# Optimization experiments

Measured on AMD Instinct MI355X. Metric: run time of the kernel, lower is better.

Reference implementation:

```python
import jax, jax.numpy as jnp
import numpy as np

B, C, H, W = 8, 6, 512, 512
N_SIGMA = 1
NUM_CLASS = 3
RES = 256
FG_W = 1.0
MAX_ID = 16  # instance ids in [0, 16); 0 is background
W_INST, W_VAR, W_SEED = 1.0, 10.0, 1.0
GAMMA = 2.0


def make_xym():
    ym = jnp.broadcast_to(jnp.linspace(0.0, H // RES, H)[None, :, None], (1, H, W))
    xm = jnp.broadcast_to(jnp.linspace(0.0, W // RES, W)[None, None, :], (1, H, W))
    return jnp.concatenate([xm, ym], 0)  # (2, H, W), channel 0 = x, 1 = y


def lovasz_hinge_flat(logits, labels_f):
    # logits, labels_f: (P,) ; labels in {0,1}
    signs = 2.0 * labels_f - 1.0
    errors = 1.0 - logits * signs
    order = jnp.argsort(-errors)  # descending
    errors_sorted = errors[order]
    gt_sorted = labels_f[order]
    gts = gt_sorted.sum()
    intersection = gts - jnp.cumsum(gt_sorted)
    union = gts + jnp.cumsum(1.0 - gt_sorted)
    jaccard = 1.0 - intersection / union
    grad = jaccard.at[1:].set(jaccard[1:] - jaccard[:-1])
    grad = jax.lax.stop_gradient(grad)
    return jnp.sum(jax.nn.relu(errors_sorted) * grad)


def focal_loss_multiclass(logits, target):
    # logits: (B, NUM_CLASS, H, W), target: (B, H, W) int class ids
    logpt = jax.nn.log_softmax(logits, axis=1)
    lp = jnp.take_along_axis(logpt, target[:, None], axis=1)[:, 0]  # (B,H,W)
    pt = jnp.exp(lp)
    return jnp.mean(-((1.0 - pt) ** GAMMA) * lp)


def setup_inputs() -> dict:
    key = jax.random.key(0)
    k1, k2, k3 = jax.random.split(key, 3)
    prediction = jax.random.normal(k1, (B, C, H, W), dtype=jnp.float32)
    labels = jax.random.randint(k2, (B, NUM_CLASS, H, W), 0, 2, dtype=jnp.int32)
    instances = jax.random.randint(k3, (B, 1, H, W), 0, MAX_ID, dtype=jnp.int32)
    return {"prediction": prediction, "labels": labels, "instances": instances}


def _loss(prediction, labels, instances):
    xym = make_xym()
    ids = jnp.arange(1, MAX_ID)

    def per_image(pred_b, inst_b, lab_b):
        spatial_emb = jnp.tanh(pred_b[0:2]) + xym           # (2,H,W)
        sigma = pred_b[2]                                    # (H,W), n_sigma=1
        seed = jax.nn.sigmoid(pred_b[2 + N_SIGMA + NUM_CLASS - 1])  # (H,W)
        label_fg = lab_b[-1]                                 # (H,W)
        bg_seed = jnp.sum(jnp.where(label_fg == 0, seed ** 2, 0.0))

        def per_id(k):
            mask = (inst_b[0] == k).astype(pred_b.dtype)     # (H,W)
            cnt = mask.sum()
            safe = jnp.maximum(cnt, 1.0)
            center = (xym * mask).sum((1, 2)) / safe         # (2,) to_center=True
            s_mean = (sigma * mask).sum() / safe
            var = (mask * (sigma - jax.lax.stop_gradient(s_mean)) ** 2).sum() / safe
            s = jnp.exp(s_mean * 10.0)
            dist = jnp.exp(-s * ((spatial_emb - center[:, None, None]) ** 2).sum(0))
            lov = lovasz_hinge_flat((dist * 2.0 - 1.0).ravel(), mask.ravel())
            seed_fg = FG_W * (mask * (seed - jax.lax.stop_gradient(dist)) ** 2).sum()
            return cnt > 0, lov, var, seed_fg

        valid, lov, var, sfg = jax.vmap(per_id)(ids)
        nobj = jnp.maximum(valid.sum().astype(pred_b.dtype), 1.0)
        inst_loss = jnp.where(valid, lov, 0.0).sum() / nobj
        var_loss = jnp.where(valid, var, 0.0).sum() / nobj
        seed_loss = (bg_seed + jnp.where(valid, sfg, 0.0).sum()) / (H * W)
        return W_INST * inst_loss + W_VAR * var_loss + W_SEED * seed_loss

    per_b = jax.vmap(per_image)(prediction, instances, labels)
    binary_closs = focal_loss_multiclass(
        prediction[:, 2 + N_SIGMA:2 + N_SIGMA + NUM_CLASS],
        jnp.argmax(labels, axis=1))
    return jnp.mean(per_b) + binary_closs


def reference(prediction, labels, instances):
    return _loss(prediction, labels, instances)
```

## Files before the change

kernel.cpp:

```cpp
#include <hip/hip_runtime.h>
#include <math.h>

#define BB 8
#define HWH (512*512)
#define NID 15
#define NSEG (BB*NID)
#define NBINS 256
#define AAF ((float)NBINS/13.0f)
#define LOG2E 1.442695041f
#define LN2 0.6931471806f
#define SLICES 128

typedef unsigned int uint32;
typedef unsigned long long uint64;

__device__ __forceinline__ float ftanh(float x){
    float t = __expf(2.0f*x);
    return 1.0f - 2.0f*__builtin_amdgcn_rcpf(t + 1.0f);
}
__device__ __forceinline__ float fsigmoid(float x){
    return __builtin_amdgcn_rcpf(1.0f + __expf(-x));
}
__device__ __forceinline__ float sconst(float x){
    return __uint_as_float(__builtin_amdgcn_readfirstlane(__float_as_uint(x)));
}

__global__ __launch_bounds__(256, 8) void phase1f(const float* __restrict__ pred,
        const int* __restrict__ labels, const int* __restrict__ inst,
        uint64* __restrict__ pstat64, float* __restrict__ pstatf,
        float* __restrict__ pstatf2,
        float* __restrict__ bgseed_p, float* __restrict__ focal_p){
    int blk = blockIdx.x;
    int b = blk >> 8;
    int t = threadIdx.x;
    int q = (blk & 255)*256 + t;

    __shared__ uint64 s64[NID];
    __shared__ float ssig[NID], ssig2[NID];
    __shared__ float wfb[4][2];
    if (t < NID){ s64[t] = 0ull; ssig[t] = 0.0f; ssig2[t] = 0.0f; }
    __syncthreads();

    const int Q = HWH/4;
    const float4* P = (const float4*)(pred + (size_t)b*6*HWH);
    const int4* L = (const int4*)(labels + (size_t)b*3*HWH);
    const int4* I = (const int4*)(inst + (size_t)b*HWH);
    float4 sg4 = P[2*Q+q], z3 = P[3*Q+q], z4 = P[4*Q+q], z5 = P[5*Q+q];
    int4 id4 = I[q];
    int4 l0 = L[q], l1 = L[Q+q], l2 = L[2*Q+q];
    int p = q*4;
    int w0 = p & 511, h0 = p >> 9;

    float facc = 0.0f, bacc = 0.0f;
    auto px = [&](float sgv, float z3v, float z4v, float z5v, int id,
                  int L0, int L1, int L2, int wv){
        float seed = fsigmoid(z5v);
        if (L2 == 0) bacc += seed*seed;
        int tc = 0, best = L0;
        if (L1 > best){ tc = 1; best = L1; }
        if (L2 > best){ tc = 2; }
        float m = fmaxf(z3v, fmaxf(z4v, z5v));
        float e3 = __expf(z3v-m), e4 = __expf(z4v-m), e5 = __expf(z5v-m);
        float sum = e3+e4+e5;
        float lse = m + __logf(sum);
        float zt = (tc==0) ? z3v : ((tc==1) ? z4v : z5v);
        float et = (tc==0) ? e3  : ((tc==1) ? e4  : e5);
        float lp = zt - lse;
        float pt = et*__builtin_amdgcn_rcpf(sum);
        float om = 1.0f - pt;
        facc -= om*om*lp;
        if (id > 0){
            atomicAdd(&s64[id-1],
                      (1ull<<42) | ((uint64)(uint32)wv<<21) | (uint64)(uint32)h0);
            atomicAdd(&ssig[id-1], sgv);
            atomicAdd(&ssig2[id-1], sgv*sgv);
        }
    };
    px(sg4.x, z3.x, z4.x, z5.x, id4.x, l0.x, l1.x, l2.x, w0);
    px(sg4.y, z3.y, z4.y, z5.y, id4.y, l0.y, l1.y, l2.y, w0+1);
    px(sg4.z, z3.z, z4.z, z5.z, id4.z, l0.z, l1.z, l2.z, w0+2);
    px(sg4.w, z3.w, z4.w, z5.w, id4.w, l0.w, l1.w, l2.w, w0+3);

    for (int o = 32; o; o >>= 1){
        facc += __shfl_xor(facc, o);
        bacc += __shfl_xor(bacc, o);
    }
    if ((t & 63) == 0){ wfb[t>>6][0] = facc; wfb[t>>6][1] = bacc; }
    __syncthreads();
    if (t < NID){
        pstat64[blk*16 + t] = s64[t];
        pstatf [blk*16 + t] = ssig[t];
        pstatf2[blk*16 + t] = ssig2[t];
    }
    if (t == 0){
        focal_p[blk]  = wfb[0][0]+wfb[1][0]+wfb[2][0]+wfb[3][0];
        bgseed_p[blk] = wfb[0][1]+wfb[1][1]+wfb[2][1]+wfb[3][1];
    }
}

__global__ __launch_bounds__(512) void phaseR(const uint64* __restrict__ pstat64,
        const float* __restrict__ pstatf, const float* __restrict__ pstatf2,
        const float* __restrict__ focal_p, const float* __restrict__ bgseed_p,
        float* __restrict__ stats, float* __restrict__ derived,
        float* __restrict__ results,
        float* __restrict__ focalR, float* __restrict__ bgseedR,
        uint32* __restrict__ Hzero, float* __restrict__ part2f){
    int b = blockIdx.x;
    int t = threadIdx.x;

    {
        const int stripe = 2*NSEG*NBINS/8;
        for (int i = b*stripe + t; i < (b+1)*stripe; i += 512) Hzero[i] = 0u;
        if (b == 0 && t < NSEG) part2f[t] = 0.0f;
    }

    int k = t & 15, chunk = t >> 4;
    float acnt = 0, asw = 0, ash = 0, af = 0, af2 = 0;
    for (int i = 0; i < 8; i++){
        int blk = b*256 + chunk*8 + i;
        uint64 v = pstat64[blk*16 + k];
        acnt += (float)(uint32)(v >> 42);
        asw  += (float)(uint32)((v >> 21) & 0x1FFFFF);
        ash  += (float)(uint32)(v & 0x1FFFFF);
        af   += pstatf[blk*16 + k];
        af2  += pstatf2[blk*16 + k];
    }
    __shared__ float tc[16], tw[16], th[16], ts[16], ts2[16];
    if (t < 16){ tc[t]=0; tw[t]=0; th[t]=0; ts[t]=0; ts2[t]=0; }
    __syncthreads();
    atomicAdd(&tc[k], acnt);
    atomicAdd(&tw[k], asw);
    atomicAdd(&th[k], ash);
    atomicAdd(&ts[k], af);
    atomicAdd(&ts2[k], af2);
    __syncthreads();
    if (t < NID){
        float cnt = tc[t];
        float safe = fmaxf(cnt, 1.0f);
        float inv = 1.0f/safe;
        const float SC = 2.0f/511.0f;
        derived[(b*NID+t)*4+0] = tw[t]*SC*inv;
        derived[(b*NID+t)*4+1] = th[t]*SC*inv;
        float sm = ts[t]*inv;
        derived[(b*NID+t)*4+2] = __expf(10.0f*sm);
        derived[(b*NID+t)*4+3] = sm;
        stats[b*60 + t*4] = cnt;
        results[(size_t)(b*NID+t)*3 + 1] = ts2[t] - cnt*sm*sm;
    }
    int w = t >> 6, lane = t & 63;
    if (w == 0){
        float f = 0;
        for (int j = 0; j < 4; j++) f += focal_p[b*256 + j*64 + lane];
        for (int o = 32; o; o >>= 1) f += __shfl_xor(f, o);
        if (lane == 0) focalR[b] = f;
    } else if (w == 1){
        float g = 0;
        for (int j = 0; j < 4; j++) g += bgseed_p[b*256 + j*64 + lane];
        for (int o = 32; o; o >>= 1) g += __shfl_xor(g, o);
        if (lane == 0) bgseedR[b] = g;
    }
}

__global__ __launch_bounds__(512, 8) void phaseLH(const float* __restrict__ pred,
        const int* __restrict__ inst, const float* __restrict__ derived,
        uint32* __restrict__ Hc, uint32* __restrict__ Hg,
        float* __restrict__ part2f){
    int idx = blockIdx.x;
    int b = idx & 7;
    int sp = idx >> 3;
    int t = threadIdx.x;
    int lane = t & 63;

    __shared__ __align__(16) uint32 hist[NID*NBINS];
    __shared__ float ssl[NID];
    __shared__ float vsB[NID];
    {
        uint4* hz = (uint4*)hist;
        for (int i = t; i < NID*NBINS/4; i += 512) hz[i] = make_uint4(0,0,0,0);
    }
    if (t < NID){
        ssl[t] = derived[(size_t)(b*NID + t)*4 + 2];
        vsB[t] = 0.0f;
    }
    float kcx[NID], kcy[NID], kcs[NID];
    #pragma unroll
    for (int j = 0; j < NID; j++){
        const float* d0 = derived + (size_t)(b*NID + j)*4;
        kcx[j] = sconst(d0[0]);
        kcy[j] = sconst(d0[1]);
        kcs[j] = sconst(LOG2E*AAF*d0[2]);
    }
    __syncthreads();

    const int Q = HWH/4;
    const int qps = Q / SLICES;
    int q0 = sp * qps;
    const float* pb = pred + (size_t)b*6*HWH;
    const float4* P0 = (const float4*)pb;
    const float4* P1 = P0 + Q;
    const float* z5p = pb + 5*HWH;
    const int4* I = (const int4*)(inst + (size_t)b*HWH);
    const float SC = 2.0f/511.0f;

    for (int q = q0 + t; q < q0 + qps; q += 512){
        int4 id4 = I[q];
        float4 a = P0[q], c = P1[q];
        int p = q*4;
        float gx = (float)(p & 511)*SC;
        float gy = (float)(p >> 9)*SC;
        auto px = [&](float av, float cv, int id, float gxv, int pi){
            float ex = ftanh(av) + gxv;
            float ey = ftanh(cv) + gy;
            int own = id - 1;
            float r2own = 0.0f;
            #pragma unroll
            for (int j = 0; j < NID; j++){
                float dx = ex - kcx[j], dy = ey - kcy[j];
                float r2 = fmaf(dx, dx, dy*dy);
                if (j == own) r2own = r2;
                float binf = fmaf(-kcs[j], r2, (float)NBINS);
                binf = fminf(fmaxf(binf, 0.0f), (float)(NBINS-1));
                int bin = (int)binf;
                bool isown = (j == own);
                bool hot = (bin == 0) && !isown;
                uint64 bal = __ballot(hot);
                if (hot){
                    if ((bal & ((1ull << lane) - 1ull)) == 0ull)
                        atomicAdd(&hist[j*NBINS],
                                  ((uint32)__popcll(bal)) << 16);
                } else if (!isown){
                    atomicAdd(&hist[j*NBINS + bin], 65536u);
                }
            }
            if (own >= 0){
                float d = __expf(-ssl[own]*r2own);
                float e = fmaf(-2.0f, d, 2.0f);
                float bf = fmaf(__log2f(e), AAF, (float)NBINS - AAF);
                bf = fminf(fmaxf(bf, 0.0f), (float)(NBINS-1));
                atomicAdd(&hist[own*NBINS + (int)bf], 65537u);
                float seed = fsigmoid(z5p[pi]);
                float sd = seed - d;
                atomicAdd(&vsB[own], sd*sd);
            }
        };
        px(a.x, c.x, id4.x, gx,      p);
        px(a.y, c.y, id4.y, gx+SC,   p+1);
        px(a.z, c.z, id4.z, gx+2*SC, p+2);
        px(a.w, c.w, id4.w, gx+3*SC, p+3);
    }
    __syncthreads();
    size_t base = (size_t)b*NID*NBINS;
    for (int i = t; i < NID*NBINS; i += 512){
        uint32 v = hist[i];
        if (v){
            uint32 cc = v >> 16, gg = v & 0xFFFFu;
            if (cc) atomicAdd(&Hc[base + i], cc);
            if (gg) atomicAdd(&Hg[base + i], gg);
        }
    }
    if (t < NID && vsB[t] != 0.0f)
        atomicAdd(&part2f[b*NID + t], vsB[t]);
}

__global__ __launch_bounds__(256) void phaseLS(const uint32* __restrict__ Hc,
        const uint32* __restrict__ Hg, const float* __restrict__ part2f,
        const float* __restrict__ stats, float* __restrict__ results){
    int idx = blockIdx.x;
    int b = idx & 7, k = idx >> 3;
    int seg = b*NID + k;
    int t = threadIdx.x;

    __shared__ uint32 wbc[4], wbg[4], wexc[4], wexg[4];
    __shared__ float wsum[4];

    size_t base = (size_t)seg*NBINS;
    uint32 cd = Hc[base + NBINS-1-t];
    uint32 gd = Hg[base + NBINS-1-t];
    uint32 ci = cd, gi2 = gd;
    int lane = t & 63, w = t >> 6;
    for (int o = 1; o < 64; o <<= 1){
        uint32 cu = __shfl_up(ci, o);
        uint32 gu = __shfl_up(gi2, o);
        if (lane >= o){ ci += cu; gi2 += gu; }
    }
    if (lane == 63){ wbc[w] = ci; wbg[w] = gi2; }
    __syncthreads();
    if (t == 0){
        uint32 rc = 0, rg = 0;
        for (int i = 0; i < 4; i++){
            uint32 a = wbc[i], bq = wbg[i];
            wexc[i] = rc; wexg[i] = rg;
            rc += a; rg += bq;
        }
    }
    __syncthreads();

    float G = stats[b*60 + k*4];
    float contrib = 0.0f;
    if (G > 0.0f && (cd | gd)){
        uint32 nb = wexc[w] + (ci - cd);
        uint32 gb = wexg[w] + (gi2 - gd);
        float jp = 0.0f;
        if (nb > 0) jp = 1.0f - (G - (float)gb)/(G + (float)(nb - gb));
        uint32 n = nb + cd, gg = gb + gd;
        float j2 = 1.0f - (G - (float)gg)/(G + (float)(n - gg));
        int bin = NBINS-1-t;
        float ev = __expf(LN2*(((float)bin + 0.5f)*(13.0f/(float)NBINS) - 12.0f));
        contrib = ev*(j2 - jp);
    }
    for (int o = 32; o; o >>= 1) contrib += __shfl_xor(contrib, o);
    if ((t & 63) == 0) wsum[w] = contrib;
    __syncthreads();
    if (t == 0){
        results[(size_t)seg*3 + 0] = wsum[0]+wsum[1]+wsum[2]+wsum[3];
        results[(size_t)seg*3 + 2] = part2f[seg];
    }
}

__global__ void phase5(const float* __restrict__ stats, const float* __restrict__ results,
                       const float* __restrict__ bgseedR, const float* __restrict__ focalR,
                       float* __restrict__ out){
    int t = threadIdx.x;
    __shared__ float per_b[BB];
    if (t < BB){
        float nvalid = 0.0f, lsum = 0.0f, vsum = 0.0f, ssum = 0.0f;
        for (int k = 0; k < NID; k++){
            int seg = t*NID + k;
            float cnt = stats[t*60 + k*4];
            if (cnt > 0.0f){
                nvalid += 1.0f;
                lsum += results[seg*3+0];
                vsum += results[seg*3+1]/cnt;
                ssum += results[seg*3+2];
            }
        }
        float nobj = fmaxf(nvalid, 1.0f);
        per_b[t] = lsum/nobj + 10.0f*(vsum/nobj) + (bgseedR[t] + ssum)/(float)HWH;
    }
    __syncthreads();
    if (t == 0){
        float s = 0.0f, fs = 0.0f;
        for (int b = 0; b < BB; b++){ s += per_b[b]; fs += focalR[b]; }
        out[0] = s/(float)BB + fs/(float)(BB*HWH);
    }
}

extern "C" void kernel_launch(void* const* d_in, const int* in_sizes, int n_in,
                              void* d_out, int out_size, void* d_ws, size_t ws_size,
                              hipStream_t stream){
    const float* pred  = (const float*)d_in[0];
    const int*   labels= (const int*)d_in[1];
    const int*   inst  = (const int*)d_in[2];
    float* out = (float*)d_out;

    uint32* Hc     = (uint32*)d_ws;
    uint32* Hg     = Hc + (size_t)NSEG*NBINS;
    float* part2f  = (float*)(Hg + (size_t)NSEG*NBINS);
    uint64* pstat64= (uint64*)(part2f + NSEG);
    float* pstatf  = (float*)(pstat64 + 2048*16);
    float* pstatf2 = pstatf + 2048*16;
    float* focal_p = pstatf2 + 2048*16;
    float* bgseed_p= focal_p + 2048;
    float* stats   = bgseed_p + 2048;
    float* derived = stats + 480;
    float* results = derived + 480;
    float* focalR  = results + 360;
    float* bgseedR = focalR + 8;

    hipLaunchKernelGGL(phase1f, dim3(2048), dim3(256), 0, stream,
                       pred, labels, inst, pstat64, pstatf, pstatf2, bgseed_p, focal_p);
    hipLaunchKernelGGL(phaseR, dim3(8), dim3(512), 0, stream,
                       pstat64, pstatf, pstatf2, focal_p, bgseed_p,
                       stats, derived, results, focalR, bgseedR, Hc, part2f);
    hipLaunchKernelGGL(phaseLH, dim3(BB*SLICES), dim3(512), 0, stream,
                       pred, inst, derived, Hc, Hg, part2f);
    hipLaunchKernelGGL(phaseLS, dim3(NSEG), dim3(256), 0, stream,
                       Hc, Hg, part2f, stats, results);
    hipLaunchKernelGGL(phase5, dim3(1), dim3(64), 0, stream,
                       stats, results, bgseedR, focalR, out);
}
```

Before: 78.46 us.

## Fuse all loss phases into one cooperative persistent kernel with grid syncs

Replaces the five-kernel launch chain with a single cooperative kernel of 512 blocks that runs the stats pass, per-segment reduction, histogram pass, Lovasz scan and final combine, separated by grid.sync. Each block keeps its loaded embedding, id and seed values in registers between the first and histogram phases, so the prediction and instance planes are not read twice. This also removes the launch gaps between kernels. In exchange it adds grid-wide barriers and needs all 512 blocks resident at once, with a fallback to the old launch chain if the cooperative launch fails. The per-segment reduction now runs on 120 blocks instead of 8.

```diff
diff --git a/kernel.cpp b/kernel.cpp
--- a/kernel.cpp
+++ b/kernel.cpp
@@ -1,5 +1,8 @@
 #include <hip/hip_runtime.h>
+#include <hip/hip_cooperative_groups.h>
 #include <math.h>
+
+namespace cg = cooperative_groups;
 
 #define BB 8
 #define HWH (512*512)
@@ -9,6 +12,8 @@
 #define AAF ((float)NBINS/13.0f)
 #define LOG2E 1.442695041f
 #define LN2 0.6931471806f
+#define NBLK 512
+#define NTHR 512
 #define SLICES 128
 
 typedef unsigned int uint32;
@@ -23,6 +28,325 @@
 }
 __device__ __forceinline__ float sconst(float x){
     return __uint_as_float(__builtin_amdgcn_readfirstlane(__float_as_uint(x)));
+}
+
+__global__ __launch_bounds__(512, 4) void mega(
+        const float* __restrict__ pred, const int* __restrict__ labels,
+        const int* __restrict__ inst,
+        uint64* __restrict__ pstat64, float* __restrict__ pstatf,
+        float* __restrict__ pstatf2,
+        float* __restrict__ focal_p, float* __restrict__ bgseed_p,
+        float* __restrict__ stats, float* __restrict__ derived,
+        float* __restrict__ results,
+        float* __restrict__ focalR, float* __restrict__ bgseedR,
+        uint32* __restrict__ Hc, uint32* __restrict__ Hg,
+        float* __restrict__ part2f, float* __restrict__ out){
+    cg::grid_group grid = cg::this_grid();
+    int blk = blockIdx.x;
+    int b = blk & 7;
+    int sp = blk >> 3;
+    int t = threadIdx.x;
+    int lane = t & 63;
+    int w = t >> 6;
+
+    __shared__ uint64 s64[NID];
+    __shared__ float ssig[NID], ssig2[NID];
+    __shared__ float wfb[8][2];
+    __shared__ __align__(16) uint32 hist[NID*NBINS];
+    __shared__ float ssl[NID], vsB[NID];
+    __shared__ uint32 wbc[8], wbg[8], wexc[8], wexg[8];
+    __shared__ float wsum[8];
+    __shared__ float red8[8];
+    __shared__ float perb[BB];
+
+    if (t < NID){ s64[t] = 0ull; ssig[t] = 0.0f; ssig2[t] = 0.0f; }
+    {
+        const int stripe = 2*NSEG*NBINS/NBLK;
+        for (int i = t; i < stripe; i += NTHR) Hc[blk*stripe + i] = 0u;
+        if (blk == 0 && t < NSEG) part2f[t] = 0.0f;
+    }
+    __syncthreads();
+
+    const int Q = HWH/4;
+    const float* pb = pred + (size_t)b*6*HWH;
+    const float4* P0 = (const float4*)pb;
+    const float4* P1 = P0 + Q;
+    const float4* P2 = P0 + 2*Q;
+    const float4* P3 = P0 + 3*Q;
+    const float4* P4 = P0 + 4*Q;
+    const float4* P5 = P0 + 5*Q;
+    const int4* Lp = (const int4*)(labels + (size_t)b*3*HWH);
+    const int4* I  = (const int4*)(inst + (size_t)b*HWH);
+    const float SC = 2.0f/511.0f;
+    int qbase = sp*1024;
+
+    float4 ra0, ra1, rc0, rc1, rs0, rs1;
+    int4 ri0, ri1;
+    float facc = 0.0f, bacc = 0.0f;
+    #pragma unroll
+    for (int it = 0; it < 2; ++it){
+        int q = qbase + it*512 + t;
+        float4 a = P0[q], c = P1[q];
+        float4 sg4 = P2[q], z3 = P3[q], z4 = P4[q], z5 = P5[q];
+        int4 id4 = I[q];
+        int4 l0 = Lp[q], l1 = Lp[Q+q], l2 = Lp[2*Q+q];
+        int p = q*4;
+        int w0 = p & 511, h0 = p >> 9;
+        auto px = [&](float sgv, float z3v, float z4v, float z5v, int id,
+                      int A0, int A1, int A2, int wv) -> float {
+            float seed = fsigmoid(z5v);
+            if (A2 == 0) bacc += seed*seed;
+            int tc = 0, best = A0;
+            if (A1 > best){ tc = 1; best = A1; }
+            if (A2 > best){ tc = 2; }
+            float m = fmaxf(z3v, fmaxf(z4v, z5v));
+            float e3 = __expf(z3v-m), e4 = __expf(z4v-m), e5 = __expf(z5v-m);
+            float sum = e3+e4+e5;
+            float lse = m + __logf(sum);
+            float zt = (tc==0) ? z3v : ((tc==1) ? z4v : z5v);
+            float et = (tc==0) ? e3  : ((tc==1) ? e4  : e5);
+            float lp = zt - lse;
+            float pt = et*__builtin_amdgcn_rcpf(sum);
+            float om = 1.0f - pt;
+            facc -= om*om*lp;
+            if (id > 0){
+                atomicAdd(&s64[id-1],
+                          (1ull<<42) | ((uint64)(uint32)wv<<21) | (uint64)(uint32)h0);
+                atomicAdd(&ssig[id-1], sgv);
+                atomicAdd(&ssig2[id-1], sgv*sgv);
+            }
+            return seed;
+        };
+        float4 seed4;
+        seed4.x = px(sg4.x, z3.x, z4.x, z5.x, id4.x, l0.x, l1.x, l2.x, w0);
+        seed4.y = px(sg4.y, z3.y, z4.y, z5.y, id4.y, l0.y, l1.y, l2.y, w0+1);
+        seed4.z = px(sg4.z, z3.z, z4.z, z5.z, id4.z, l0.z, l1.z, l2.z, w0+2);
+        seed4.w = px(sg4.w, z3.w, z4.w, z5.w, id4.w, l0.w, l1.w, l2.w, w0+3);
+        if (it == 0){ ra0 = a; rc0 = c; ri0 = id4; rs0 = seed4; }
+        else        { ra1 = a; rc1 = c; ri1 = id4; rs1 = seed4; }
+    }
+    for (int o = 32; o; o >>= 1){
+        facc += __shfl_xor(facc, o);
+        bacc += __shfl_xor(bacc, o);
+    }
+    if (lane == 0){ wfb[w][0] = facc; wfb[w][1] = bacc; }
+    __syncthreads();
+    if (t < NID){
+        pstat64[blk*16 + t] = s64[t];
+        pstatf [blk*16 + t] = ssig[t];
+        pstatf2[blk*16 + t] = ssig2[t];
+    }
+    if (t == 0){
+        float f = 0.0f, g = 0.0f;
+        for (int i = 0; i < 8; i++){ f += wfb[i][0]; g += wfb[i][1]; }
+        focal_p[blk] = f; bgseed_p[blk] = g;
+    }
+
+    grid.sync();
+
+    if (blk < NSEG){
+        int bb = blk & 7, k = blk >> 3;
+        if (t < 64){
+            uint64 v = pstat64[(size_t)(bb + 8*t)*16 + k];
+            float acnt = (float)(uint32)(v >> 42);
+            float asw  = (float)(uint32)((v >> 21) & 0x1FFFFF);
+            float ash  = (float)(uint32)(v & 0x1FFFFF);
+            float af   = pstatf [(bb + 8*t)*16 + k];
+            float af2  = pstatf2[(bb + 8*t)*16 + k];
+            for (int o = 32; o; o >>= 1){
+                acnt += __shfl_xor(acnt, o);
+                asw  += __shfl_xor(asw,  o);
+                ash  += __shfl_xor(ash,  o);
+                af   += __shfl_xor(af,   o);
+                af2  += __shfl_xor(af2,  o);
+            }
+            if (lane == 0){
+                float cnt = acnt;
+                float safe = fmaxf(cnt, 1.0f);
+                float inv = 1.0f/safe;
+                int seg = bb*NID + k;
+                derived[seg*4+0] = asw*SC*inv;
+                derived[seg*4+1] = ash*SC*inv;
+                float sm = af*inv;
+                derived[seg*4+2] = __expf(10.0f*sm);
+                derived[seg*4+3] = sm;
+                stats[bb*60 + k*4] = cnt;
+                results[(size_t)seg*3 + 1] = af2 - cnt*sm*sm;
+            }
+        }
+    } else if (blk == NSEG){
+        if (t < 8) red8[t] = 0.0f;
+        __syncthreads();
+        atomicAdd(&red8[t & 7], bgseed_p[t]);
+        float f = focal_p[t];
+        for (int o = 32; o; o >>= 1) f += __shfl_xor(f, o);
+        if (lane == 0) wsum[w] = f;
+        __syncthreads();
+        if (t < 8) bgseedR[t] = red8[t];
+        if (t == 0){
+            float fs = 0.0f;
+            for (int i = 0; i < 8; i++) fs += wsum[i];
+            focalR[0] = fs;
+        }
+    }
+
+    grid.sync();
+
+    {
+        uint4* hz = (uint4*)hist;
+        for (int i = t; i < NID*NBINS/4; i += NTHR) hz[i] = make_uint4(0,0,0,0);
+    }
+    if (t < NID){
+        ssl[t] = derived[(size_t)(b*NID + t)*4 + 2];
+        vsB[t] = 0.0f;
+    }
+    float kcx[NID], kcy[NID], kcs[NID];
+    #pragma unroll
+    for (int j = 0; j < NID; j++){
+        const float* d0 = derived + (size_t)(b*NID + j)*4;
+        kcx[j] = sconst(d0[0]);
+        kcy[j] = sconst(d0[1]);
+        kcs[j] = sconst(LOG2E*AAF*d0[2]);
+    }
+    __syncthreads();
+
+    auto pc = [&](float av, float cv, int id, float gxv, float gy, float seed){
+        float ex = ftanh(av) + gxv;
+        float ey = ftanh(cv) + gy;
+        int own = id - 1;
+        float r2own = 0.0f;
+        #pragma unroll
+        for (int j = 0; j < NID; j++){
+            float dx = ex - kcx[j], dy = ey - kcy[j];
+            float r2 = fmaf(dx, dx, dy*dy);
+            if (j == own) r2own = r2;
+            float binf = fmaf(-kcs[j], r2, (float)NBINS);
+            binf = fminf(fmaxf(binf, 0.0f), (float)(NBINS-1));
+            int bin = (int)binf;
+            bool isown = (j == own);
+            bool hot = (bin == 0) && !isown;
+            uint64 bal = __ballot(hot);
+            if (hot){
+                if ((bal & ((1ull << lane) - 1ull)) == 0ull)
+                    atomicAdd(&hist[j*NBINS], ((uint32)__popcll(bal)) << 16);
+            } else if (!isown){
+                atomicAdd(&hist[j*NBINS + bin], 65536u);
+            }
+        }
+        if (own >= 0){
+            float d = __expf(-ssl[own]*r2own);
+            float e = fmaf(-2.0f, d, 2.0f);
+            float bf = fmaf(__log2f(e), AAF, (float)NBINS - AAF);
+            bf = fminf(fmaxf(bf, 0.0f), (float)(NBINS-1));
+            atomicAdd(&hist[own*NBINS + (int)bf], 65537u);
+            float sd = seed - d;
+            atomicAdd(&vsB[own], sd*sd);
+        }
+    };
+    {
+        int q0 = qbase + t, q1 = qbase + 512 + t;
+        int p0 = q0*4, p1 = q1*4;
+        float gx0 = (float)(p0 & 511)*SC, gy0 = (float)(p0 >> 9)*SC;
+        float gx1 = (float)(p1 & 511)*SC, gy1 = (float)(p1 >> 9)*SC;
+        pc(ra0.x, rc0.x, ri0.x, gx0,        gy0, rs0.x);
+        pc(ra0.y, rc0.y, ri0.y, gx0+SC,     gy0, rs0.y);
+        pc(ra0.z, rc0.z, ri0.z, gx0+2*SC,   gy0, rs0.z);
+        pc(ra0.w, rc0.w, ri0.w, gx0+3*SC,   gy0, rs0.w);
+        pc(ra1.x, rc1.x, ri1.x, gx1,        gy1, rs1.x);
+        pc(ra1.y, rc1.y, ri1.y, gx1+SC,     gy1, rs1.y);
+        pc(ra1.z, rc1.z, ri1.z, gx1+2*SC,   gy1, rs1.z);
+        pc(ra1.w, rc1.w, ri1.w, gx1+3*SC,   gy1, rs1.w);
+    }
+    __syncthreads();
+    {
+        size_t hbase = (size_t)b*NID*NBINS;
+        for (int i = t; i < NID*NBINS; i += NTHR){
+            uint32 v = hist[i];
+            if (v){
+                uint32 cc = v >> 16, gg = v & 0xFFFFu;
+                if (cc) atomicAdd(&Hc[hbase + i], cc);
+                if (gg) atomicAdd(&Hg[hbase + i], gg);
+            }
+        }
+        if (t < NID && vsB[t] != 0.0f)
+            atomicAdd(&part2f[b*NID + t], vsB[t]);
+    }
+
+    grid.sync();
+
+    if (blk < NSEG){
+        int bb = blk & 7, k = blk >> 3;
+        int seg = bb*NID + k;
+        uint32 cd = 0, gd = 0;
+        if (t < 256){
+            size_t base = (size_t)seg*NBINS;
+            cd = Hc[base + NBINS-1-t];
+            gd = Hg[base + NBINS-1-t];
+        }
+        uint32 ci = cd, gi2 = gd;
+        for (int o = 1; o < 64; o <<= 1){
+            uint32 cu = __shfl_up(ci, o);
+            uint32 gu = __shfl_up(gi2, o);
+            if (lane >= o){ ci += cu; gi2 += gu; }
+        }
+        if (lane == 63){ wbc[w] = ci; wbg[w] = gi2; }
+        __syncthreads();
+        if (t == 0){
+            uint32 rc2 = 0, rg2 = 0;
+            for (int i = 0; i < 4; i++){
+                uint32 aa = wbc[i], bq = wbg[i];
+                wexc[i] = rc2; wexg[i] = rg2;
+                rc2 += aa; rg2 += bq;
+            }
+        }
+        __syncthreads();
+        float G = stats[bb*60 + k*4];
+        float contrib = 0.0f;
+        if (t < 256 && G > 0.0f && (cd | gd)){
+            uint32 nb = wexc[w] + (ci - cd);
+            uint32 gb = wexg[w] + (gi2 - gd);
+            float jp = 0.0f;
+            if (nb > 0) jp = 1.0f - (G - (float)gb)/(G + (float)(nb - gb));
+            uint32 n = nb + cd, gg = gb + gd;
+            float j2 = 1.0f - (G - (float)gg)/(G + (float)(n - gg));
+            int bin = NBINS-1-t;
+            float ev = __expf(LN2*(((float)bin + 0.5f)*(13.0f/(float)NBINS) - 12.0f));
+            contrib = ev*(j2 - jp);
+        }
+        for (int o = 32; o; o >>= 1) contrib += __shfl_xor(contrib, o);
+        if (lane == 0) wsum[w] = contrib;
+        __syncthreads();
+        if (t == 0){
+            results[(size_t)seg*3 + 0] = wsum[0]+wsum[1]+wsum[2]+wsum[3];
+            results[(size_t)seg*3 + 2] = part2f[seg];
+        }
+    }
+
+    grid.sync();
+
+    if (blk == 0){
+        if (t < BB){
+            float nvalid = 0.0f, lsum = 0.0f, vsum = 0.0f, ssum = 0.0f;
+            for (int k = 0; k < NID; k++){
+                int seg = t*NID + k;
+                float cnt = stats[t*60 + k*4];
+                if (cnt > 0.0f){
+                    nvalid += 1.0f;
+                    lsum += results[seg*3+0];
+                    vsum += results[seg*3+1]/cnt;
+                    ssum += results[seg*3+2];
+                }
+            }
+            float nobj = fmaxf(nvalid, 1.0f);
+            perb[t] = lsum/nobj + 10.0f*(vsum/nobj) + (bgseedR[t] + ssum)/(float)HWH;
+        }
+        __syncthreads();
+        if (t == 0){
+            float s = 0.0f;
+            for (int bq = 0; bq < BB; bq++) s += perb[bq];
+            out[0] = s/(float)BB + focalR[0]/(float)(BB*HWH);
+        }
+    }
 }
 
 __global__ __launch_bounds__(256, 8) void phase1f(const float* __restrict__ pred,
@@ -107,13 +431,11 @@
         uint32* __restrict__ Hzero, float* __restrict__ part2f){
     int b = blockIdx.x;
     int t = threadIdx.x;
-
     {
         const int stripe = 2*NSEG*NBINS/8;
         for (int i = b*stripe + t; i < (b+1)*stripe; i += 512) Hzero[i] = 0u;
         if (b == 0 && t < NSEG) part2f[t] = 0.0f;
     }
-
     int k = t & 15, chunk = t >> 4;
     float acnt = 0, asw = 0, ash = 0, af = 0, af2 = 0;
     for (int i = 0; i < 8; i++){
@@ -356,7 +678,7 @@
     uint32* Hc     = (uint32*)d_ws;
     uint32* Hg     = Hc + (size_t)NSEG*NBINS;
     float* part2f  = (float*)(Hg + (size_t)NSEG*NBINS);
-    uint64* pstat64= (uint64*)(part2f + NSEG);
+    uint64* pstat64= (uint64*)(part2f + 128);
     float* pstatf  = (float*)(pstat64 + 2048*16);
     float* pstatf2 = pstatf + 2048*16;
     float* focal_p = pstatf2 + 2048*16;
@@ -367,15 +689,26 @@
     float* focalR  = results + 360;
     float* bgseedR = focalR + 8;
 
-    hipLaunchKernelGGL(phase1f, dim3(2048), dim3(256), 0, stream,
-                       pred, labels, inst, pstat64, pstatf, pstatf2, bgseed_p, focal_p);
-    hipLaunchKernelGGL(phaseR, dim3(8), dim3(512), 0, stream,
-                       pstat64, pstatf, pstatf2, focal_p, bgseed_p,
-                       stats, derived, results, focalR, bgseedR, Hc, part2f);
-    hipLaunchKernelGGL(phaseLH, dim3(BB*SLICES), dim3(512), 0, stream,
-                       pred, inst, derived, Hc, Hg, part2f);
-    hipLaunchKernelGGL(phaseLS, dim3(NSEG), dim3(256), 0, stream,
-                       Hc, Hg, part2f, stats, results);
-    hipLaunchKernelGGL(phase5, dim3(1), dim3(64), 0, stream,
-                       stats, results, bgseedR, focalR, out);
-}
+    void* args[] = { (void*)&pred, (void*)&labels, (void*)&inst,
+                     (void*)&pstat64, (void*)&pstatf, (void*)&pstatf2,
+                     (void*)&focal_p, (void*)&bgseed_p,
+                     (void*)&stats, (void*)&derived, (void*)&results,
+                     (void*)&focalR, (void*)&bgseedR,
+                     (void*)&Hc, (void*)&Hg, (void*)&part2f, (void*)&out };
+    hipError_t err = hipLaunchCooperativeKernel((void*)mega, dim3(NBLK), dim3(NTHR),
+                                                args, 0, stream);
+    if (err != hipSuccess){
+        hipLaunchKernelGGL(phase1f, dim3(2048), dim3(256), 0, stream,
+                           pred, labels, inst, pstat64, pstatf, pstatf2,
+                           bgseed_p, focal_p);
+        hipLaunchKernelGGL(phaseR, dim3(8), dim3(512), 0, stream,
+                           pstat64, pstatf, pstatf2, focal_p, bgseed_p,
+                           stats, derived, results, focalR, bgseedR, Hc, part2f);
+        hipLaunchKernelGGL(phaseLH, dim3(BB*SLICES), dim3(512), 0, stream,
+                           pred, inst, derived, Hc, Hg, part2f);
+        hipLaunchKernelGGL(phaseLS, dim3(NSEG), dim3(256), 0, stream,
+                           Hc, Hg, part2f, stats, results);
+        hipLaunchKernelGGL(phase5, dim3(1), dim3(64), 0, stream,
+                           stats, results, bgseedR, focalR, out);
+    }
+}
```

Result: slower. 289.1 us (+268.4%).
